# Kernel optimization log

Hardware: AMD Instinct MI355X
Metric: run time of the kernel (lower is better)

The kernel has to match this reference:

```python
import jax, jax.numpy as jnp
import numpy as np

BATCH, SIZE_IN, SIZE_OUT = 2048, 256, 512


def setup_inputs() -> dict:
    key = jax.random.key(0)
    kx, ka = jax.random.split(key)
    x = jax.random.normal(kx, (BATCH, SIZE_IN), dtype=jnp.float32)
    A = jax.random.normal(ka, (SIZE_IN, SIZE_OUT), dtype=jnp.float32)
    return {"x": x, "A": A}


def reference(x, A):
    # W = sigmoid(A): [size_in, size_out]
    W = jax.nn.sigmoid(A)
    # tropical (max-times) matmul: out[i,k] = max_j W[j,k] * x[i,j]
    # broadcast [B,1,J_in->axis1]... x: [B,J,1], W: [1,J,K] -> [B,J,K] -> max over J
    out = jnp.max(x[:, :, None] * W[None, :, :], axis=1)  # [B, K]
    return out
```

## Files before the change

### kernel.cpp

```cpp
#include <hip/hip_runtime.h>


constexpr int JD = 256;
constexpr int KD = 512;
constexpr int TI = 4;
constexpr int ROWS = 16;
constexpr int NCH = 16;

typedef _Float16 h1;
typedef __attribute__((ext_vector_type(2))) _Float16 h2v;
typedef __attribute__((ext_vector_type(4))) float f4;
typedef __attribute__((ext_vector_type(2))) float f2;

__device__ __forceinline__ float sigmoidf_fast(float a) {
    return 1.0f / (1.0f + __expf(-a));
}

__global__ __launch_bounds__(256) void wpack(const float* __restrict__ A,
                                             h2v* __restrict__ Wp) {
    const int t  = blockIdx.x * 256 + threadIdx.x;
    const int p  = t >> 7;
    const int kq = (t & 127) << 2;
    const f4 a0 = *(const f4*)&A[(2 * p) * KD + kq];
    const f4 a1 = *(const f4*)&A[(2 * p + 1) * KD + kq];
    union { f4 v; h2v h[4]; } u;
    #pragma unroll
    for (int q = 0; q < 4; ++q)
        u.h[q] = h2v{(h1)sigmoidf_fast(a0[q]), (h1)sigmoidf_fast(a1[q])};
    *(f4*)&Wp[p * KD + kq] = u.v;
}

__global__ __launch_bounds__(256) void tropical_mm_kernel(
        const float* __restrict__ x,
        const h2v* __restrict__ Wp,
        float* __restrict__ out) {
    __shared__ h2v xl[ROWS][JD / 2];

    const int t    = (int)threadIdx.x;
    const int lane = t & 63;
    const int wv   = __builtin_amdgcn_readfirstlane(t >> 6);
    const int bk   = (int)blockIdx.x & 3;
    const int bi   = (int)blockIdx.x >> 2;
    const int i0   = bi * ROWS;
    const int k    = bk * 128 + 2 * lane;

    {
        const int srow = t >> 4;
        const float* xs = x + (i0 + srow) * JD + (t & 15) * 16;
        f4 f0 = ((const f4*)xs)[0];
        f4 f1 = ((const f4*)xs)[1];
        f4 f2_ = ((const f4*)xs)[2];
        f4 f3 = ((const f4*)xs)[3];
        union { f4 v; h2v h[4]; } u0, u1;
        u0.h[0] = h2v{(h1)f0.x, (h1)f0.y};
        u0.h[1] = h2v{(h1)f0.z, (h1)f0.w};
        u0.h[2] = h2v{(h1)f1.x, (h1)f1.y};
        u0.h[3] = h2v{(h1)f1.z, (h1)f1.w};
        u1.h[0] = h2v{(h1)f2_.x, (h1)f2_.y};
        u1.h[1] = h2v{(h1)f2_.z, (h1)f2_.w};
        u1.h[2] = h2v{(h1)f3.x, (h1)f3.y};
        u1.h[3] = h2v{(h1)f3.z, (h1)f3.w};
        *(f4*)&xl[srow][(t & 15) * 8]     = u0.v;
        *(f4*)&xl[srow][(t & 15) * 8 + 4] = u1.v;
    }
    __syncthreads();

    const h2v* Wk = Wp + k;
    const int r0 = wv * TI;

    h2v acc[TI][2];
    #pragma unroll
    for (int r = 0; r < TI; ++r) {
        acc[r][0] = h2v{(h1)(-65504.0f), (h1)(-65504.0f)};
        acc[r][1] = acc[r][0];
    }

    union wpair { f2 v; h2v h[2]; };
    wpair WA[8], WB[8];
    f4 XA[TI][2], XB[TI][2];

    auto loadW = [&](wpair (&W)[8], int c) {
        const h2v* p = Wk + (c * 8) * KD;
        #pragma unroll
        for (int q = 0; q < 8; ++q) W[q].v = *(const f2*)&p[q * KD];
    };
    auto loadX = [&](f4 (&X)[TI][2], int c) {
        #pragma unroll
        for (int r = 0; r < TI; ++r) {
            X[r][0] = *(const f4*)&xl[r0 + r][c * 8];
            X[r][1] = *(const f4*)&xl[r0 + r][c * 8 + 4];
        }
    };
    auto compute = [&](const f4 (&X)[TI][2], const wpair (&W)[8]) {
        #pragma unroll
        for (int r = 0; r < TI; ++r) {
            #pragma unroll
            for (int hf = 0; hf < 2; ++hf) {
                union { f4 v; h2v h[4]; } u;
                u.v = X[r][hf];
                #pragma unroll
                for (int q = 0; q < 4; ++q) {
                    const h2v xp = u.h[q];
                    const wpair w = W[hf * 4 + q];
                    acc[r][0] = __builtin_elementwise_max(acc[r][0], xp * w.h[0]);
                    acc[r][1] = __builtin_elementwise_max(acc[r][1], xp * w.h[1]);
                }
            }
        }
    };

    loadW(WA, 0);
    loadX(XA, 0);

    #pragma unroll 1
    for (int c = 0; c < NCH; c += 2) {
        loadW(WB, c + 1);
        loadX(XB, c + 1);
        compute(XA, WA);
        if (c + 2 < NCH) {
            loadW(WA, c + 2);
            loadX(XA, c + 2);
        }
        compute(XB, WB);
    }

    #pragma unroll
    for (int r = 0; r < TI; ++r) {
        f2 o;
        o.x = fmaxf((float)acc[r][0][0], (float)acc[r][0][1]);
        o.y = fmaxf((float)acc[r][1][0], (float)acc[r][1][1]);
        *(f2*)&out[(i0 + r0 + r) * KD + k] = o;
    }
}

extern "C" void kernel_launch(void* const* d_in, const int* in_sizes, int n_in,
                              void* d_out, int out_size, void* d_ws, size_t ws_size,
                              hipStream_t stream) {
    const float* x = (const float*)d_in[0];
    const float* A = (const float*)d_in[1];
    float* out = (float*)d_out;
    h2v* Wp = (h2v*)d_ws;

    hipLaunchKernelGGL(wpack, dim3(64), dim3(256), 0, stream, A, Wp);

    hipLaunchKernelGGL(tropical_mm_kernel, dim3(512), dim3(256), 0, stream,
                       x, Wp, out);
}
```

Measured before the change: 23.19 us.

## Stage transposed W tile in LDS and read weights from shared memory

Each block now loads its 128-column slice of packed W into padded LDS, transposed so each k column's j-pairs are contiguous. Compute then reads W with 16-byte LDS loads instead of per-row global 8-byte loads. Output columns are remapped to lane and lane+64, which gives coalesced scalar stores. The cost is about 67KB of LDS per block, which lowers occupancy, plus a strided scalar global gather before the barrier.

```diff
diff --git a/kernel.cpp b/kernel.cpp
--- a/kernel.cpp
+++ b/kernel.cpp
@@ -1,16 +1,17 @@
 #include <hip/hip_runtime.h>
 
 
-constexpr int JD = 256;
-constexpr int KD = 512;
-constexpr int TI = 4;
+constexpr int JD   = 256;
+constexpr int KD   = 512;
+constexpr int TI   = 4;
 constexpr int ROWS = 16;
-constexpr int NCH = 16;
+constexpr int KW   = 128;
+constexpr int NCH  = 16;
+constexpr int LSTR = 132;
 
 typedef _Float16 h1;
 typedef __attribute__((ext_vector_type(2))) _Float16 h2v;
 typedef __attribute__((ext_vector_type(4))) float f4;
-typedef __attribute__((ext_vector_type(2))) float f2;
 
 __device__ __forceinline__ float sigmoidf_fast(float a) {
     return 1.0f / (1.0f + __expf(-a));
@@ -34,7 +35,8 @@
         const float* __restrict__ x,
         const h2v* __restrict__ Wp,
         float* __restrict__ out) {
-    __shared__ h2v xl[ROWS][JD / 2];
+    __shared__ h2v Wl[KW * LSTR];
+    __shared__ h2v xl[ROWS * LSTR];
 
     const int t    = (int)threadIdx.x;
     const int lane = t & 63;
@@ -42,11 +44,12 @@
     const int bk   = (int)blockIdx.x & 3;
     const int bi   = (int)blockIdx.x >> 2;
     const int i0   = bi * ROWS;
-    const int k    = bk * 128 + 2 * lane;
+    const int k0   = bk * KW;
 
     {
         const int srow = t >> 4;
-        const float* xs = x + (i0 + srow) * JD + (t & 15) * 16;
+        const int c16  = t & 15;
+        const float* xs = x + (i0 + srow) * JD + c16 * 16;
         f4 f0 = ((const f4*)xs)[0];
         f4 f1 = ((const f4*)xs)[1];
         f4 f2_ = ((const f4*)xs)[2];
@@ -60,12 +63,27 @@
         u1.h[1] = h2v{(h1)f2_.z, (h1)f2_.w};
         u1.h[2] = h2v{(h1)f3.x, (h1)f3.y};
         u1.h[3] = h2v{(h1)f3.z, (h1)f3.w};
-        *(f4*)&xl[srow][(t & 15) * 8]     = u0.v;
-        *(f4*)&xl[srow][(t & 15) * 8 + 4] = u1.v;
+        *(f4*)&xl[srow * LSTR + c16 * 8]     = u0.v;
+        *(f4*)&xl[srow * LSTR + c16 * 8 + 4] = u1.v;
+    }
+
+    {
+        const int kl = t & 127;
+        const int pb = (t >> 7) * 64;
+        const h2v* src = Wp + k0 + kl;
+        #pragma unroll 4
+        for (int pass = 0; pass < 16; ++pass) {
+            const int p0 = pb + pass * 4;
+            union { f4 v; h2v h[4]; } u;
+            u.h[0] = src[(p0 + 0) * KD];
+            u.h[1] = src[(p0 + 1) * KD];
+            u.h[2] = src[(p0 + 2) * KD];
+            u.h[3] = src[(p0 + 3) * KD];
+            *(f4*)&Wl[kl * LSTR + p0] = u.v;
+        }
     }
     __syncthreads();
 
-    const h2v* Wk = Wp + k;
     const int r0 = wv * TI;
 
     h2v acc[TI][2];
@@ -75,61 +93,62 @@
         acc[r][1] = acc[r][0];
     }
 
-    union wpair { f2 v; h2v h[2]; };
-    wpair WA[8], WB[8];
     f4 XA[TI][2], XB[TI][2];
+    f4 WA[2][2], WB[2][2];
 
-    auto loadW = [&](wpair (&W)[8], int c) {
-        const h2v* p = Wk + (c * 8) * KD;
-        #pragma unroll
-        for (int q = 0; q < 8; ++q) W[q].v = *(const f2*)&p[q * KD];
-    };
     auto loadX = [&](f4 (&X)[TI][2], int c) {
         #pragma unroll
         for (int r = 0; r < TI; ++r) {
-            X[r][0] = *(const f4*)&xl[r0 + r][c * 8];
-            X[r][1] = *(const f4*)&xl[r0 + r][c * 8 + 4];
+            X[r][0] = *(const f4*)&xl[(r0 + r) * LSTR + c * 8];
+            X[r][1] = *(const f4*)&xl[(r0 + r) * LSTR + c * 8 + 4];
         }
     };
-    auto compute = [&](const f4 (&X)[TI][2], const wpair (&W)[8]) {
+    auto loadW = [&](f4 (&W)[2][2], int c) {
+        W[0][0] = *(const f4*)&Wl[lane * LSTR + c * 8];
+        W[0][1] = *(const f4*)&Wl[lane * LSTR + c * 8 + 4];
+        W[1][0] = *(const f4*)&Wl[(64 + lane) * LSTR + c * 8];
+        W[1][1] = *(const f4*)&Wl[(64 + lane) * LSTR + c * 8 + 4];
+    };
+    auto compute = [&](const f4 (&X)[TI][2], const f4 (&W)[2][2]) {
         #pragma unroll
         for (int r = 0; r < TI; ++r) {
             #pragma unroll
             for (int hf = 0; hf < 2; ++hf) {
-                union { f4 v; h2v h[4]; } u;
-                u.v = X[r][hf];
+                union { f4 v; h2v h[4]; } ux, uw0, uw1;
+                ux.v  = X[r][hf];
+                uw0.v = W[0][hf];
+                uw1.v = W[1][hf];
                 #pragma unroll
                 for (int q = 0; q < 4; ++q) {
-                    const h2v xp = u.h[q];
-                    const wpair w = W[hf * 4 + q];
-                    acc[r][0] = __builtin_elementwise_max(acc[r][0], xp * w.h[0]);
-                    acc[r][1] = __builtin_elementwise_max(acc[r][1], xp * w.h[1]);
+                    acc[r][0] = __builtin_elementwise_max(acc[r][0],
+                                                          ux.h[q] * uw0.h[q]);
+                    acc[r][1] = __builtin_elementwise_max(acc[r][1],
+                                                          ux.h[q] * uw1.h[q]);
                 }
             }
         }
     };
 
+    loadX(XA, 0);
     loadW(WA, 0);
-    loadX(XA, 0);
 
     #pragma unroll 1
     for (int c = 0; c < NCH; c += 2) {
+        loadX(XB, c + 1);
         loadW(WB, c + 1);
-        loadX(XB, c + 1);
         compute(XA, WA);
         if (c + 2 < NCH) {
+            loadX(XA, c + 2);
             loadW(WA, c + 2);
-            loadX(XA, c + 2);
         }
         compute(XB, WB);
     }
 
     #pragma unroll
     for (int r = 0; r < TI; ++r) {
-        f2 o;
-        o.x = fmaxf((float)acc[r][0][0], (float)acc[r][0][1]);
-        o.y = fmaxf((float)acc[r][1][0], (float)acc[r][1][1]);
-        *(f2*)&out[(i0 + r0 + r) * KD + k] = o;
+        const int row = (i0 + r0 + r) * KD + k0;
+        out[row + lane]      = fmaxf((float)acc[r][0][0], (float)acc[r][0][1]);
+        out[row + 64 + lane] = fmaxf((float)acc[r][1][0], (float)acc[r][1][1]);
     }
 }
 
```

Measured after the change: 24.91 us. +7.4%, slower.
